# Kernel tuning notes

Measured on AMD Instinct MI355X. Metric: run time of the kernel, lower is better.

## Reference

```python
import jax, jax.numpy as jnp
import numpy as np

S = 8192        # seq_length
H2 = 1024       # 2 * lstm_hidden_size
A = 2048        # attention_hidden_size
E = 768         # embedding_dim == pos_embedding_dim


def _bahdanau_weights(sentence, length, ctx, W_s, b_s, W_c, b_c, v, b_v):
    # sentence: [1, S, H2], ctx: [1, E_ctx]
    u = jnp.einsum('bsh,ha->bsa', sentence, W_s) + b_s \
        + (ctx @ W_c + b_c)[:, None, :]                    # [1, S, A]
    e = jnp.einsum('bsa,a->bs', jnp.tanh(u), v) + b_v       # [1, S]
    mask = jnp.arange(S)[None, :] >= length[:, None]        # [1, S] key mask
    e = jnp.where(mask, -jnp.inf, e)
    all_inf = jnp.all(mask, axis=1)                         # [1]
    # guard fully-masked rows so softmax stays finite, then zero them (matches torch)
    e_safe = jnp.where(all_inf[:, None], jnp.zeros_like(e), e)
    w = jax.nn.softmax(e_safe, axis=1)
    return jnp.where(all_inf[:, None], 0.0, w)              # [1, S]


def setup_inputs() -> dict:
    key = jax.random.key(0)
    ks = jax.random.split(key, 24)
    f = jax.random.normal
    sc_s = 1.0 / np.sqrt(H2)
    sc_c = 1.0 / np.sqrt(E)
    sc_v = 1.0 / np.sqrt(A)
    inp = {
        'sentence': f(ks[0], (1, S, H2), jnp.float32),
        'length': jax.random.randint(ks[1], (1,), 0, S),
        'pos_embedding': f(ks[2], (1, E), jnp.float32),
        'cardinal_phrase_embedding': f(ks[3], (1, E), jnp.float32),
        'headline_embedding': f(ks[4], (1, E), jnp.float32),
    }
    i = 5
    for tag in ('p', 'c', 'h'):
        inp[f'W_sent_{tag}'] = f(ks[i], (H2, A), jnp.float32) * sc_s; i += 1
        inp[f'b_sent_{tag}'] = f(ks[i], (A,), jnp.float32) * sc_s; i += 1
        inp[f'W_ctx_{tag}'] = f(ks[i], (E, A), jnp.float32) * sc_c; i += 1
        inp[f'b_ctx_{tag}'] = f(ks[i], (A,), jnp.float32) * sc_c; i += 1
        inp[f'v_{tag}'] = f(ks[i], (A,), jnp.float32) * sc_v; i += 1
        inp[f'bv_{tag}'] = f(ks[i], (), jnp.float32) * sc_v; i += 1
    return inp


def reference(sentence, length, pos_embedding, cardinal_phrase_embedding,
              headline_embedding,
              W_sent_p, b_sent_p, W_ctx_p, b_ctx_p, v_p, bv_p,
              W_sent_c, b_sent_c, W_ctx_c, b_ctx_c, v_c, bv_c,
              W_sent_h, b_sent_h, W_ctx_h, b_ctx_h, v_h, bv_h):
    w_pos = _bahdanau_weights(sentence, length, pos_embedding,
                              W_sent_p, b_sent_p, W_ctx_p, b_ctx_p, v_p, bv_p)
    w_card = _bahdanau_weights(sentence, length, cardinal_phrase_embedding,
                               W_sent_c, b_sent_c, W_ctx_c, b_ctx_c, v_c, bv_c)
    w_head = _bahdanau_weights(sentence, length, headline_embedding,
                               W_sent_h, b_sent_h, W_ctx_h, b_ctx_h, v_h, bv_h)
    fused = (w_pos + w_card + w_head) / 3.0                 # [1, S]
    return jnp.einsum('bs,bsh->bh', fused, sentence)        # [1, H2]
```

## Files before the change

### kernel.cpp

```cpp
#include <hip/hip_runtime.h>
#include <hip/hip_bf16.h>
#include <stdint.h>


namespace {

constexpr int S = 8192;
constexpr int H = 1024;
constexpr int A = 2048;
constexpr int E = 768;

typedef __bf16 bf16x8 __attribute__((ext_vector_type(8)));
typedef float f32x4 __attribute__((ext_vector_type(4)));

__device__ __forceinline__ void gl_lds16(const void* g, void* l) {
  __builtin_amdgcn_global_load_lds(
      (const __attribute__((address_space(1))) void*)g,
      (__attribute__((address_space(3))) void*)l, 16, 0, 0);
}

__global__ __launch_bounds__(256)
void k_prep(const float* __restrict__ sentence, __bf16* __restrict__ sentB,
            const float* __restrict__ Wp, const float* __restrict__ Wc_s,
            const float* __restrict__ Wh, __bf16* __restrict__ WtB,
            const float* __restrict__ ctx_p, const float* __restrict__ ctx_c,
            const float* __restrict__ ctx_h,
            const float* __restrict__ Wcx_p, const float* __restrict__ Wcx_c,
            const float* __restrict__ Wcx_h,
            const float* __restrict__ bs_p, const float* __restrict__ bs_c,
            const float* __restrict__ bs_h,
            const float* __restrict__ bc_p, const float* __restrict__ bc_c,
            const float* __restrict__ bc_h,
            float* __restrict__ ctxb_q, float* __restrict__ e_arr,
            const int* __restrict__ length, float* __restrict__ out, int n_out) {
  __shared__ float tile[64][65];
  int b = blockIdx.x;
  int t = threadIdx.x;

  if (b < 4096) {
    int len = min(max(length[0], 0), S);
    int lenp = (len + 63) & ~63;
    if (b * 2 >= lenp) return;
    int g = b * 256 + t;
    const float4* s4 = (const float4*)sentence + (size_t)g * 2;
    float4 a = s4[0], c = s4[1];
    bf16x8 o;
    o[0] = (__bf16)a.x; o[1] = (__bf16)a.y; o[2] = (__bf16)a.z; o[3] = (__bf16)a.w;
    o[4] = (__bf16)c.x; o[5] = (__bf16)c.y; o[6] = (__bf16)c.z; o[7] = (__bf16)c.w;
    *((bf16x8*)sentB + g) = o;
  } else if (b < 5632) {
    int r = b - 4096;
    int head = r >> 9; r &= 511;
    const float* W = head == 0 ? Wp : (head == 1 ? Wc_s : Wh);
    __bf16* dst = WtB + (size_t)head * A * H;
    int a0 = (r & 31) * 64;
    int k0 = (r >> 5) * 64;
#pragma unroll
    for (int i = 0; i < 8; ++i) {
      int idx = t + i * 256;
      int rr = idx >> 5;
      int cc = (idx & 31) * 2;
      float2 w2 = *(const float2*)&W[(size_t)(k0 + rr) * A + a0 + cc];
      tile[cc][rr] = w2.x;
      tile[cc + 1][rr] = w2.y;
    }
    __syncthreads();
#pragma unroll
    for (int i = 0; i < 8; ++i) {
      int idx = t + i * 256;
      int al = idx >> 5;
      int kl = (idx & 31) * 2;
      union { ushort2 u; __bf16 h[2]; } o;
      o.h[0] = (__bf16)tile[al][kl];
      o.h[1] = (__bf16)tile[al][kl + 1];
      *(ushort2*)&dst[(size_t)(a0 + al) * H + k0 + kl] = o.u;
    }
  } else if (b < 5728) {
    int r = b - 5632;
    int head = r >> 5;
    int sub = r & 31;
    int ablk = sub & 7;
    int eq = sub >> 3;
    const float* ctx = head == 0 ? ctx_p : (head == 1 ? ctx_c : ctx_h);
    const float* Wc  = head == 0 ? Wcx_p : (head == 1 ? Wcx_c : Wcx_h);
    int a = ablk * 256 + t;
    float s = 0.f;
    if (eq == 0) {
      const float* bs = head == 0 ? bs_p : (head == 1 ? bs_c : bs_h);
      const float* bc = head == 0 ? bc_p : (head == 1 ? bc_c : bc_h);
      s = bs[a] + bc[a];
    }
    int e0 = eq * 192;
#pragma unroll 8
    for (int e = e0; e < e0 + 192; ++e) s = fmaf(ctx[e], Wc[(size_t)e * A + a], s);
    ctxb_q[eq * 3 * A + head * A + a] = s;
  } else {
    int idx = (b - 5728) * 256 + t;
    float4 z = {0.f, 0.f, 0.f, 0.f};
    int total = 6144 + (n_out >> 2);
    for (int i = idx; i < total; i += 2048) {
      if (i < 6144) ((float4*)e_arr)[i] = z;
      else ((float4*)out)[i - 6144] = z;
    }
  }
}

__global__ __launch_bounds__(256)
void k_gemm_e(const __bf16* __restrict__ sentB, const __bf16* __restrict__ WtB,
              const float* __restrict__ ctxb_q,
              const float* __restrict__ v_p, const float* __restrict__ v_c,
              const float* __restrict__ v_h,
              const int* __restrict__ length, float* __restrict__ e_out) {
  int bid = blockIdx.x;
  int xcd = bid & 7;
  int j = bid >> 3;
  int mt = j / 6;
  int pl = j - mt * 6;
  int panel = xcd * 6 + pl;
  int n0 = (panel & 15) * 128;
  int head = panel >> 4;

  int m0 = mt * 64;
  int len = min(max(length[0], 0), S);
  if (m0 >= len) return;
  const float* v  = head == 0 ? v_p : (head == 1 ? v_c : v_h);
  const __bf16* Wt = WtB + (size_t)head * A * H;
  float* e_h = e_out + head * S;

  __shared__ __align__(16) __bf16 lsA[3 * 2048];
  __shared__ __align__(16) __bf16 lsB[3 * 4096];
  __shared__ float e_part[64];

  int tid = threadIdx.x;
  if (tid < 64) e_part[tid] = 0.f;

  int lane = tid & 63;
  int wave = tid >> 6;
  int wm = wave >> 1, wn = wave & 1;
  int quad = lane >> 4, l16 = lane & 15;

  f32x4 acc[2][4];
#pragma unroll
  for (int i = 0; i < 2; ++i)
#pragma unroll
    for (int j2 = 0; j2 < 4; ++j2) acc[i][j2] = (f32x4){0.f, 0.f, 0.f, 0.f};

  const __bf16* gA0 = sentB + (size_t)(m0 + (tid >> 2)) * H + ((tid & 3) * 8);
  const __bf16* gB0 = Wt + (size_t)(n0 + (tid >> 2)) * H + ((tid & 3) * 8);
  const __bf16* gB1 = gB0 + (size_t)64 * H;

#define STAGE(bufi, kk)                                           \
  do {                                                            \
    gl_lds16(gA0 + (kk), lsA + (bufi) * 2048 + tid * 8);          \
    gl_lds16(gB0 + (kk), lsB + (bufi) * 4096 + tid * 8);          \
    gl_lds16(gB1 + (kk), lsB + (bufi) * 4096 + 2048 + tid * 8);   \
  } while (0)

#define COMPUTE(bufi)                                                                          \
  do {                                                                                         \
    bf16x8 af[2], bfv[4];                                                                      \
    _Pragma("unroll")                                                                          \
    for (int i = 0; i < 2; ++i)                                                                \
      af[i] = *(const bf16x8*)&lsA[(bufi) * 2048 + (wm * 32 + i * 16 + l16) * 32 + quad * 8];  \
    _Pragma("unroll")                                                                          \
    for (int jj = 0; jj < 4; ++jj)                                                             \
      bfv[jj] = *(const bf16x8*)&lsB[(bufi) * 4096 + (wn * 64 + jj * 16 + l16) * 32 + quad * 8]; \
    _Pragma("unroll")                                                                          \
    for (int i = 0; i < 2; ++i)                                                                \
      _Pragma("unroll")                                                                        \
      for (int jj = 0; jj < 4; ++jj)                                                           \
        acc[i][jj] = __builtin_amdgcn_mfma_f32_16x16x32_bf16(af[i], bfv[jj], acc[i][jj], 0, 0, 0);\
  } while (0)

  STAGE(0, 0);
  STAGE(1, 32);
  int cur = 0, pf = 2;
#pragma unroll 1
  for (int t = 0; t < 31; ++t) {
    asm volatile("s_waitcnt vmcnt(3)");
    __builtin_amdgcn_s_barrier();
    __builtin_amdgcn_sched_barrier(0);
    if (t < 30) STAGE(pf, (t + 2) * 32);
    COMPUTE(cur);
    cur = cur == 2 ? 0 : cur + 1;
    pf = pf == 2 ? 0 : pf + 1;
  }
  asm volatile("s_waitcnt vmcnt(0)");
  __builtin_amdgcn_s_barrier();
  __builtin_amdgcn_sched_barrier(0);
  COMPUTE(cur);

#undef STAGE
#undef COMPUTE

  float vj[4], cbj[4];
#pragma unroll
  for (int j2 = 0; j2 < 4; ++j2) {
    int col = n0 + wn * 64 + j2 * 16 + l16;
    vj[j2] = v[col];
    cbj[j2] = ctxb_q[head * A + col] + ctxb_q[3 * A + head * A + col] +
              ctxb_q[6 * A + head * A + col] + ctxb_q[9 * A + head * A + col];
  }
#pragma unroll
  for (int i = 0; i < 2; ++i) {
#pragma unroll
    for (int r = 0; r < 4; ++r) {
      float p = 0.f;
#pragma unroll
      for (int j2 = 0; j2 < 4; ++j2) {
        float u = acc[i][j2][r] + cbj[j2];
        float ex = __expf(2.f * u);
        float th = 1.f - 2.f / (ex + 1.f);
        p = fmaf(th, vj[j2], p);
      }
      p += __shfl_xor(p, 1);
      p += __shfl_xor(p, 2);
      p += __shfl_xor(p, 4);
      p += __shfl_xor(p, 8);
      if (l16 == 0) atomicAdd(&e_part[wm * 32 + i * 16 + quad * 4 + r], p);
    }
  }
  __syncthreads();
  if (tid < 64) atomicAdd(&e_h[m0 + tid], e_part[tid]);
}

__global__ void k_stats(const float* __restrict__ e_arr, const int* __restrict__ length,
                        float* __restrict__ stats) {
  int head = blockIdx.x;
  const float* e_h = e_arr + head * S;
  int len = min(max(length[0], 0), S);
  int tid = threadIdx.x;
  __shared__ float red[4];
  __shared__ float bmax;

  float m = -3.4e38f;
  for (int s = tid; s < len; s += 256) m = fmaxf(m, e_h[s]);
#pragma unroll
  for (int o = 32; o >= 1; o >>= 1) m = fmaxf(m, __shfl_xor(m, o));
  if ((tid & 63) == 0) red[tid >> 6] = m;
  __syncthreads();
  if (tid == 0) bmax = fmaxf(fmaxf(red[0], red[1]), fmaxf(red[2], red[3]));
  __syncthreads();
  float mm = bmax;

  float ss = 0.f;
  for (int s = tid; s < len; s += 256) ss += __expf(e_h[s] - mm);
#pragma unroll
  for (int o = 32; o >= 1; o >>= 1) ss += __shfl_xor(ss, o);
  __syncthreads();
  if ((tid & 63) == 0) red[tid >> 6] = ss;
  __syncthreads();
  if (tid == 0) {
    stats[head * 2 + 0] = mm;
    stats[head * 2 + 1] = red[0] + red[1] + red[2] + red[3];
  }
}

__global__ void k_out(const float* __restrict__ sent, const float* __restrict__ e_arr,
                      const float* __restrict__ stats, const int* __restrict__ length,
                      float* __restrict__ out) {
  int len = min(max(length[0], 0), S);
  int r0 = blockIdx.x * 16;
  if (r0 >= len) return;
  int tid = threadIdx.x;

  __shared__ float wrow[16];
  if (tid < 16 && r0 + tid < len) {
    int r = r0 + tid;
    wrow[tid] = (__expf(e_arr[r] - stats[0]) / stats[1] +
                 __expf(e_arr[S + r] - stats[2]) / stats[3] +
                 __expf(e_arr[2 * S + r] - stats[4]) / stats[5]) * (1.f / 3.f);
  }
  __syncthreads();

  int col = tid * 4;
  int rend = min(r0 + 16, len);
  float4 acc = {0.f, 0.f, 0.f, 0.f};
  for (int r = r0; r < rend; ++r) {
    float w = wrow[r - r0];
    float4 x = *(const float4*)(sent + (size_t)r * H + col);
    acc.x = fmaf(w, x.x, acc.x);
    acc.y = fmaf(w, x.y, acc.y);
    acc.z = fmaf(w, x.z, acc.z);
    acc.w = fmaf(w, x.w, acc.w);
  }
  atomicAdd(&out[col + 0], acc.x);
  atomicAdd(&out[col + 1], acc.y);
  atomicAdd(&out[col + 2], acc.z);
  atomicAdd(&out[col + 3], acc.w);
}

}

extern "C" void kernel_launch(void* const* d_in, const int* in_sizes, int n_in,
                              void* d_out, int out_size, void* d_ws, size_t ws_size,
                              hipStream_t stream) {
  const float* sentence = (const float*)d_in[0];
  const int* length     = (const int*)d_in[1];
  const float* ctx_p = (const float*)d_in[2];
  const float* ctx_c = (const float*)d_in[3];
  const float* ctx_h = (const float*)d_in[4];
  const float* W_s[3] = {(const float*)d_in[5],  (const float*)d_in[11], (const float*)d_in[17]};
  const float* b_s[3] = {(const float*)d_in[6],  (const float*)d_in[12], (const float*)d_in[18]};
  const float* W_c[3] = {(const float*)d_in[7],  (const float*)d_in[13], (const float*)d_in[19]};
  const float* b_c[3] = {(const float*)d_in[8],  (const float*)d_in[14], (const float*)d_in[20]};
  const float* v_[3]  = {(const float*)d_in[9],  (const float*)d_in[15], (const float*)d_in[21]};
  float* out = (float*)d_out;

  char* ws = (char*)d_ws;
  __bf16* sentB  = (__bf16*)(ws);
  __bf16* WtB    = (__bf16*)(ws + 16777216);
  float* ctxb_q  = (float*)(ws + 29360128);
  float* e_arr   = (float*)(ws + 29458432);
  float* stats   = (float*)(ws + 29556736);

  k_prep<<<5736, 256, 0, stream>>>(sentence, sentB,
                                   W_s[0], W_s[1], W_s[2], WtB,
                                   ctx_p, ctx_c, ctx_h,
                                   W_c[0], W_c[1], W_c[2],
                                   b_s[0], b_s[1], b_s[2],
                                   b_c[0], b_c[1], b_c[2], ctxb_q, e_arr,
                                   length, out, out_size);
  k_gemm_e<<<6144, 256, 0, stream>>>(sentB, WtB, ctxb_q,
                                     v_[0], v_[1], v_[2], length, e_arr);
  k_stats<<<3, 256, 0, stream>>>(e_arr, length, stats);
  k_out<<<S / 16, 256, 0, stream>>>(sentence, e_arr, stats, length, out);
}
```

Before: 213.5 us.

## Stage GEMM tiles through registers into padded LDS rows

Replaces the direct global-to-LDS async loads with ordinary global loads into registers, followed by explicit LDS stores. The LDS row stride goes from 32 to 40 bf16 elements, a padding meant to cut bank conflicts on the MFMA fragment reads. The K loop is unrolled by three with three register slots to keep global loads in flight one stage ahead. In exchange it uses more VGPRs and LDS and adds extra LDS write instructions, which may reduce occupancy or overlap.

Result: no change. 210.5 us (-1.4%).

```diff
diff --git a/kernel.cpp b/kernel.cpp
--- a/kernel.cpp
+++ b/kernel.cpp
@@ -12,12 +12,6 @@
 
 typedef __bf16 bf16x8 __attribute__((ext_vector_type(8)));
 typedef float f32x4 __attribute__((ext_vector_type(4)));
-
-__device__ __forceinline__ void gl_lds16(const void* g, void* l) {
-  __builtin_amdgcn_global_load_lds(
-      (const __attribute__((address_space(1))) void*)g,
-      (__attribute__((address_space(3))) void*)l, 16, 0, 0);
-}
 
 __global__ __launch_bounds__(256)
 void k_prep(const float* __restrict__ sentence, __bf16* __restrict__ sentB,
@@ -127,8 +121,8 @@
   const __bf16* Wt = WtB + (size_t)head * A * H;
   float* e_h = e_out + head * S;
 
-  __shared__ __align__(16) __bf16 lsA[3 * 2048];
-  __shared__ __align__(16) __bf16 lsB[3 * 4096];
+  __shared__ __align__(16) __bf16 lsA[3 * 2560];
+  __shared__ __align__(16) __bf16 lsB[3 * 5120];
   __shared__ float e_part[64];
 
   int tid = threadIdx.x;
@@ -149,49 +143,76 @@
   const __bf16* gB0 = Wt + (size_t)(n0 + (tid >> 2)) * H + ((tid & 3) * 8);
   const __bf16* gB1 = gB0 + (size_t)64 * H;
 
-#define STAGE(bufi, kk)                                           \
-  do {                                                            \
-    gl_lds16(gA0 + (kk), lsA + (bufi) * 2048 + tid * 8);          \
-    gl_lds16(gB0 + (kk), lsB + (bufi) * 4096 + tid * 8);          \
-    gl_lds16(gB1 + (kk), lsB + (bufi) * 4096 + 2048 + tid * 8);   \
+  int wA  = (tid >> 2) * 40 + (tid & 3) * 8;
+  int wB0 = wA;
+  int wB1 = wA + 64 * 40;
+
+  uint4 s0A, s0B0, s0B1, s1A, s1B0, s1B1, s2A, s2B0, s2B1;
+
+#define LOADB(sl, kk)                             \
+  do {                                            \
+    sl##A  = *(const uint4*)(gA0 + (kk));         \
+    sl##B0 = *(const uint4*)(gB0 + (kk));         \
+    sl##B1 = *(const uint4*)(gB1 + (kk));         \
   } while (0)
 
-#define COMPUTE(bufi)                                                                          \
-  do {                                                                                         \
-    bf16x8 af[2], bfv[4];                                                                      \
-    _Pragma("unroll")                                                                          \
-    for (int i = 0; i < 2; ++i)                                                                \
-      af[i] = *(const bf16x8*)&lsA[(bufi) * 2048 + (wm * 32 + i * 16 + l16) * 32 + quad * 8];  \
-    _Pragma("unroll")                                                                          \
-    for (int jj = 0; jj < 4; ++jj)                                                             \
-      bfv[jj] = *(const bf16x8*)&lsB[(bufi) * 4096 + (wn * 64 + jj * 16 + l16) * 32 + quad * 8]; \
-    _Pragma("unroll")                                                                          \
-    for (int i = 0; i < 2; ++i)                                                                \
-      _Pragma("unroll")                                                                        \
-      for (int jj = 0; jj < 4; ++jj)                                                           \
+#define WRITEB(sl, bufi)                          \
+  do {                                            \
+    *(uint4*)&lsA[(bufi) * 2560 + wA]  = sl##A;   \
+    *(uint4*)&lsB[(bufi) * 5120 + wB0] = sl##B0;  \
+    *(uint4*)&lsB[(bufi) * 5120 + wB1] = sl##B1;  \
+  } while (0)
+
+#define COMPUTE(bufi)                                                                           \
+  do {                                                                                          \
+    bf16x8 af[2], bfv[4];                                                                       \
+    _Pragma("unroll")                                                                           \
+    for (int i = 0; i < 2; ++i)                                                                 \
+      af[i] = *(const bf16x8*)&lsA[(bufi) * 2560 + (wm * 32 + i * 16 + l16) * 40 + quad * 8];   \
+    _Pragma("unroll")                                                                           \
+    for (int jj = 0; jj < 4; ++jj)                                                              \
+      bfv[jj] = *(const bf16x8*)&lsB[(bufi) * 5120 + (wn * 64 + jj * 16 + l16) * 40 + quad * 8];\
+    _Pragma("unroll")                                                                           \
+    for (int i = 0; i < 2; ++i)                                                                 \
+      _Pragma("unroll")                                                                         \
+      for (int jj = 0; jj < 4; ++jj)                                                            \
         acc[i][jj] = __builtin_amdgcn_mfma_f32_16x16x32_bf16(af[i], bfv[jj], acc[i][jj], 0, 0, 0);\
   } while (0)
 
-  STAGE(0, 0);
-  STAGE(1, 32);
-  int cur = 0, pf = 2;
-#pragma unroll 1
-  for (int t = 0; t < 31; ++t) {
-    asm volatile("s_waitcnt vmcnt(3)");
-    __builtin_amdgcn_s_barrier();
-    __builtin_amdgcn_sched_barrier(0);
-    if (t < 30) STAGE(pf, (t + 2) * 32);
-    COMPUTE(cur);
-    cur = cur == 2 ? 0 : cur + 1;
-    pf = pf == 2 ? 0 : pf + 1;
-  }
-  asm volatile("s_waitcnt vmcnt(0)");
+#define ITER(t, sc, bc, sw, bw)                                 \
+  do {                                                          \
+    COMPUTE(bc);                                                \
+    if ((t) <= 28) LOADB(sc, ((t) + 3) * 32);                   \
+    WRITEB(sw, bw);                                             \
+    asm volatile("s_waitcnt lgkmcnt(0)");                       \
+    __builtin_amdgcn_sched_barrier(0);                          \
+    __builtin_amdgcn_s_barrier();                               \
+    __builtin_amdgcn_sched_barrier(0);                          \
+  } while (0)
+
+  LOADB(s0, 0);
+  LOADB(s1, 32);
+  LOADB(s2, 64);
+  WRITEB(s0, 0);
+  WRITEB(s1, 1);
+  asm volatile("s_waitcnt lgkmcnt(0)");
+  __builtin_amdgcn_sched_barrier(0);
   __builtin_amdgcn_s_barrier();
   __builtin_amdgcn_sched_barrier(0);
-  COMPUTE(cur);
-
-#undef STAGE
+
+#pragma unroll 1
+  for (int t = 0; t < 30; t += 3) {
+    ITER(t + 0, s0, 0, s2, 2);
+    ITER(t + 1, s1, 1, s0, 0);
+    ITER(t + 2, s2, 2, s1, 1);
+  }
+  COMPUTE(0);
+  COMPUTE(1);
+
+#undef LOADB
+#undef WRITEB
 #undef COMPUTE
+#undef ITER
 
   float vj[4], cbj[4];
 #pragma unroll
```

## Fuse sentence fp32-to-bf16 conversion into GEMM A-operand loads

Applied to the files above, without the earlier changes.

Removes the separate sentence-to-bf16 conversion pass from the prep kernel and its workspace buffer. The GEMM now loads fp32 sentence rows straight into registers, converts them to bf16 fragments in-loop, and feeds the MFMAs directly, while B still streams through LDS with a 3-buffer pipeline unrolled by 6. This drops a full write and re-read of a 16MB bf16 copy. In exchange each of the 6144 GEMM blocks reads fp32 A (twice the bytes) redundantly across the 48 N-panels, and register pressure rises.

Measured after the change: 270.6 us. 26.7% more time.

```diff
diff --git a/kernel.cpp b/kernel.cpp
--- a/kernel.cpp
+++ b/kernel.cpp
@@ -19,9 +19,15 @@
       (__attribute__((address_space(3))) void*)l, 16, 0, 0);
 }
 
+__device__ __forceinline__ bf16x8 cvt8(float4 lo, float4 hi) {
+  bf16x8 r;
+  r[0] = (__bf16)lo.x; r[1] = (__bf16)lo.y; r[2] = (__bf16)lo.z; r[3] = (__bf16)lo.w;
+  r[4] = (__bf16)hi.x; r[5] = (__bf16)hi.y; r[6] = (__bf16)hi.z; r[7] = (__bf16)hi.w;
+  return r;
+}
+
 __global__ __launch_bounds__(256)
-void k_prep(const float* __restrict__ sentence, __bf16* __restrict__ sentB,
-            const float* __restrict__ Wp, const float* __restrict__ Wc_s,
+void k_prep(const float* __restrict__ Wp, const float* __restrict__ Wc_s,
             const float* __restrict__ Wh, __bf16* __restrict__ WtB,
             const float* __restrict__ ctx_p, const float* __restrict__ ctx_c,
             const float* __restrict__ ctx_h,
@@ -32,24 +38,13 @@
             const float* __restrict__ bc_p, const float* __restrict__ bc_c,
             const float* __restrict__ bc_h,
             float* __restrict__ ctxb_q, float* __restrict__ e_arr,
-            const int* __restrict__ length, float* __restrict__ out, int n_out) {
+            float* __restrict__ out, int n_out) {
   __shared__ float tile[64][65];
   int b = blockIdx.x;
   int t = threadIdx.x;
 
-  if (b < 4096) {
-    int len = min(max(length[0], 0), S);
-    int lenp = (len + 63) & ~63;
-    if (b * 2 >= lenp) return;
-    int g = b * 256 + t;
-    const float4* s4 = (const float4*)sentence + (size_t)g * 2;
-    float4 a = s4[0], c = s4[1];
-    bf16x8 o;
-    o[0] = (__bf16)a.x; o[1] = (__bf16)a.y; o[2] = (__bf16)a.z; o[3] = (__bf16)a.w;
-    o[4] = (__bf16)c.x; o[5] = (__bf16)c.y; o[6] = (__bf16)c.z; o[7] = (__bf16)c.w;
-    *((bf16x8*)sentB + g) = o;
-  } else if (b < 5632) {
-    int r = b - 4096;
+  if (b < 1536) {
+    int r = b;
     int head = r >> 9; r &= 511;
     const float* W = head == 0 ? Wp : (head == 1 ? Wc_s : Wh);
     __bf16* dst = WtB + (size_t)head * A * H;
@@ -75,8 +70,8 @@
       o.h[1] = (__bf16)tile[al][kl + 1];
       *(ushort2*)&dst[(size_t)(a0 + al) * H + k0 + kl] = o.u;
     }
-  } else if (b < 5728) {
-    int r = b - 5632;
+  } else if (b < 1632) {
+    int r = b - 1536;
     int head = r >> 5;
     int sub = r & 31;
     int ablk = sub & 7;
@@ -95,7 +90,7 @@
     for (int e = e0; e < e0 + 192; ++e) s = fmaf(ctx[e], Wc[(size_t)e * A + a], s);
     ctxb_q[eq * 3 * A + head * A + a] = s;
   } else {
-    int idx = (b - 5728) * 256 + t;
+    int idx = (b - 1632) * 256 + t;
     float4 z = {0.f, 0.f, 0.f, 0.f};
     int total = 6144 + (n_out >> 2);
     for (int i = idx; i < total; i += 2048) {
@@ -106,7 +101,7 @@
 }
 
 __global__ __launch_bounds__(256)
-void k_gemm_e(const __bf16* __restrict__ sentB, const __bf16* __restrict__ WtB,
+void k_gemm_e(const float* __restrict__ sent, const __bf16* __restrict__ WtB,
               const float* __restrict__ ctxb_q,
               const float* __restrict__ v_p, const float* __restrict__ v_c,
               const float* __restrict__ v_h,
@@ -127,7 +122,6 @@
   const __bf16* Wt = WtB + (size_t)head * A * H;
   float* e_h = e_out + head * S;
 
-  __shared__ __align__(16) __bf16 lsA[3 * 2048];
   __shared__ __align__(16) __bf16 lsB[3 * 4096];
   __shared__ float e_part[64];
 
@@ -145,53 +139,92 @@
 #pragma unroll
     for (int j2 = 0; j2 < 4; ++j2) acc[i][j2] = (f32x4){0.f, 0.f, 0.f, 0.f};
 
-  const __bf16* gA0 = sentB + (size_t)(m0 + (tid >> 2)) * H + ((tid & 3) * 8);
   const __bf16* gB0 = Wt + (size_t)(n0 + (tid >> 2)) * H + ((tid & 3) * 8);
   const __bf16* gB1 = gB0 + (size_t)64 * H;
-
-#define STAGE(bufi, kk)                                           \
+  const float* gA0 = sent + (size_t)(m0 + wm * 32 + l16) * H + quad * 8;
+  const float* gA1 = gA0 + (size_t)16 * H;
+
+  float4 s0[4], s1[4];
+  bf16x8 ab0, ab1;
+
+#define AISSUE(sl, kk)                              \
+  do {                                              \
+    sl[0] = *(const float4*)(gA0 + (kk));           \
+    sl[1] = *(const float4*)(gA0 + (kk) + 4);       \
+    sl[2] = *(const float4*)(gA1 + (kk));           \
+    sl[3] = *(const float4*)(gA1 + (kk) + 4);       \
+  } while (0)
+
+#define BISSUE(bufi, kk)                                          \
   do {                                                            \
-    gl_lds16(gA0 + (kk), lsA + (bufi) * 2048 + tid * 8);          \
     gl_lds16(gB0 + (kk), lsB + (bufi) * 4096 + tid * 8);          \
     gl_lds16(gB1 + (kk), lsB + (bufi) * 4096 + 2048 + tid * 8);   \
   } while (0)
 
-#define COMPUTE(bufi)                                                                          \
-  do {                                                                                         \
-    bf16x8 af[2], bfv[4];                                                                      \
-    _Pragma("unroll")                                                                          \
-    for (int i = 0; i < 2; ++i)                                                                \
-      af[i] = *(const bf16x8*)&lsA[(bufi) * 2048 + (wm * 32 + i * 16 + l16) * 32 + quad * 8];  \
-    _Pragma("unroll")                                                                          \
-    for (int jj = 0; jj < 4; ++jj)                                                             \
-      bfv[jj] = *(const bf16x8*)&lsB[(bufi) * 4096 + (wn * 64 + jj * 16 + l16) * 32 + quad * 8]; \
-    _Pragma("unroll")                                                                          \
-    for (int i = 0; i < 2; ++i)                                                                \
-      _Pragma("unroll")                                                                        \
-      for (int jj = 0; jj < 4; ++jj)                                                           \
-        acc[i][jj] = __builtin_amdgcn_mfma_f32_16x16x32_bf16(af[i], bfv[jj], acc[i][jj], 0, 0, 0);\
-  } while (0)
-
-  STAGE(0, 0);
-  STAGE(1, 32);
-  int cur = 0, pf = 2;
-#pragma unroll 1
-  for (int t = 0; t < 31; ++t) {
-    asm volatile("s_waitcnt vmcnt(3)");
-    __builtin_amdgcn_s_barrier();
-    __builtin_amdgcn_sched_barrier(0);
-    if (t < 30) STAGE(pf, (t + 2) * 32);
-    COMPUTE(cur);
-    cur = cur == 2 ? 0 : cur + 1;
-    pf = pf == 2 ? 0 : pf + 1;
-  }
-  asm volatile("s_waitcnt vmcnt(0)");
+#define ACVT(sl)                                    \
+  do {                                              \
+    ab0 = cvt8(sl[0], sl[1]);                       \
+    ab1 = cvt8(sl[2], sl[3]);                       \
+  } while (0)
+
+#define COMPUTE(bufi)                                                                           \
+  do {                                                                                          \
+    bf16x8 bfv[4];                                                                              \
+    _Pragma("unroll")                                                                           \
+    for (int jj = 0; jj < 4; ++jj)                                                              \
+      bfv[jj] = *(const bf16x8*)&lsB[(bufi) * 4096 + (wn * 64 + jj * 16 + l16) * 32 + quad * 8];\
+    _Pragma("unroll")                                                                           \
+    for (int jj = 0; jj < 4; ++jj) {                                                            \
+      acc[0][jj] = __builtin_amdgcn_mfma_f32_16x16x32_bf16(ab0, bfv[jj], acc[0][jj], 0, 0, 0);  \
+      acc[1][jj] = __builtin_amdgcn_mfma_f32_16x16x32_bf16(ab1, bfv[jj], acc[1][jj], 0, 0, 0);  \
+    }                                                                                           \
+  } while (0)
+
+#define ITER(t, sIss, sCvt, bufC, bufN)             \
+  do {                                              \
+    AISSUE(sIss, ((t) + 2) * 32);                   \
+    BISSUE(bufN, ((t) + 2) * 32);                   \
+    COMPUTE(bufC);                                  \
+    asm volatile("s_waitcnt vmcnt(6)");             \
+    ACVT(sCvt);                                     \
+    __builtin_amdgcn_sched_barrier(0);              \
+    __builtin_amdgcn_s_barrier();                   \
+    __builtin_amdgcn_sched_barrier(0);              \
+  } while (0)
+
+  AISSUE(s0, 0);
+  BISSUE(0, 0);
+  AISSUE(s1, 32);
+  BISSUE(1, 32);
+  asm volatile("s_waitcnt vmcnt(6)");
+  ACVT(s0);
+  __builtin_amdgcn_sched_barrier(0);
   __builtin_amdgcn_s_barrier();
   __builtin_amdgcn_sched_barrier(0);
-  COMPUTE(cur);
-
-#undef STAGE
+
+#pragma unroll 1
+  for (int r = 0; r < 5; ++r) {
+    int tb = r * 6;
+    ITER(tb + 0, s0, s1, 0, 2);
+    ITER(tb + 1, s1, s0, 1, 0);
+    ITER(tb + 2, s0, s1, 2, 1);
+    ITER(tb + 3, s1, s0, 0, 2);
+    ITER(tb + 4, s0, s1, 1, 0);
+    ITER(tb + 5, s1, s0, 2, 1);
+  }
+  COMPUTE(0);
+  asm volatile("s_waitcnt vmcnt(0)");
+  ACVT(s1);
+  __builtin_amdgcn_sched_barrier(0);
+  __builtin_amdgcn_s_barrier();
+  __builtin_amdgcn_sched_barrier(0);
+  COMPUTE(1);
+
+#undef AISSUE
+#undef BISSUE
+#undef ACVT
 #undef COMPUTE
+#undef ITER
 
   float vj[4], cbj[4];
 #pragma unroll
@@ -308,20 +341,18 @@
   float* out = (float*)d_out;
 
   char* ws = (char*)d_ws;
-  __bf16* sentB  = (__bf16*)(ws);
-  __bf16* WtB    = (__bf16*)(ws + 16777216);
-  float* ctxb_q  = (float*)(ws + 29360128);
-  float* e_arr   = (float*)(ws + 29458432);
-  float* stats   = (float*)(ws + 29556736);
-
-  k_prep<<<5736, 256, 0, stream>>>(sentence, sentB,
-                                   W_s[0], W_s[1], W_s[2], WtB,
+  __bf16* WtB    = (__bf16*)(ws);
+  float* ctxb_q  = (float*)(ws + 12582912);
+  float* e_arr   = (float*)(ws + 12681216);
+  float* stats   = (float*)(ws + 12779520);
+
+  k_prep<<<1640, 256, 0, stream>>>(W_s[0], W_s[1], W_s[2], WtB,
                                    ctx_p, ctx_c, ctx_h,
                                    W_c[0], W_c[1], W_c[2],
                                    b_s[0], b_s[1], b_s[2],
                                    b_c[0], b_c[1], b_c[2], ctxb_q, e_arr,
-                                   length, out, out_size);
-  k_gemm_e<<<6144, 256, 0, stream>>>(sentB, WtB, ctxb_q,
+                                   out, out_size);
+  k_gemm_e<<<6144, 256, 0, stream>>>(sentence, WtB, ctxb_q,
                                      v_[0], v_[1], v_[2], length, e_arr);
   k_stats<<<3, 256, 0, stream>>>(e_arr, length, stats);
   k_out<<<S / 16, 256, 0, stream>>>(sentence, e_arr, stats, length, out);
```

## Pre-pack sentence into MFMA fragment layout and load A operand directly to registers

Applied to the files above, without the earlier changes.

The prep kernel now writes the bf16 sentence in a layout that matches the MFMA A-fragments for each 32-row group and k-tile. The GEMM kernel drops the A tile from shared memory and loads A fragments straight from global memory into registers, using a three-slot register rotation. The main loop is unrolled by three with explicit waitcnt and barrier placement. This removes LDS traffic and LDS reads for A, and shrinks shared memory, at the cost of more VGPRs and uncoalesced-looking but contiguous per-wave global loads. The pipelining behaviour depends on the vmcnt accounting being correct for the mix of register loads and LDS-direct loads.

After: 213.5 us. No clear change (+0.0%).

```diff
diff --git a/kernel.cpp b/kernel.cpp
--- a/kernel.cpp
+++ b/kernel.cpp
@@ -20,7 +20,7 @@
 }
 
 __global__ __launch_bounds__(256)
-void k_prep(const float* __restrict__ sentence, __bf16* __restrict__ sentB,
+void k_prep(const float* __restrict__ sentence, __bf16* __restrict__ packA,
             const float* __restrict__ Wp, const float* __restrict__ Wc_s,
             const float* __restrict__ Wh, __bf16* __restrict__ WtB,
             const float* __restrict__ ctx_p, const float* __restrict__ ctx_c,
@@ -40,14 +40,18 @@
   if (b < 4096) {
     int len = min(max(length[0], 0), S);
     int lenp = (len + 63) & ~63;
-    if (b * 2 >= lenp) return;
-    int g = b * 256 + t;
-    const float4* s4 = (const float4*)sentence + (size_t)g * 2;
-    float4 a = s4[0], c = s4[1];
+    int row = b * 2 + (t >> 7);
+    if (row >= lenp) return;
+    int chunk = t & 127;
+    const float4* s4 = (const float4*)(sentence + (size_t)row * H + chunk * 8);
+    float4 lo = s4[0], hi = s4[1];
     bf16x8 o;
-    o[0] = (__bf16)a.x; o[1] = (__bf16)a.y; o[2] = (__bf16)a.z; o[3] = (__bf16)a.w;
-    o[4] = (__bf16)c.x; o[5] = (__bf16)c.y; o[6] = (__bf16)c.z; o[7] = (__bf16)c.w;
-    *((bf16x8*)sentB + g) = o;
+    o[0] = (__bf16)lo.x; o[1] = (__bf16)lo.y; o[2] = (__bf16)lo.z; o[3] = (__bf16)lo.w;
+    o[4] = (__bf16)hi.x; o[5] = (__bf16)hi.y; o[6] = (__bf16)hi.z; o[7] = (__bf16)hi.w;
+    int g = row >> 5, f = (row >> 4) & 1, l16 = row & 15;
+    int kt = chunk >> 2, quad = chunk & 3;
+    size_t dst = ((size_t)((g * 32 + kt) * 2 + f)) * 512 + (quad * 16 + l16) * 8;
+    *(bf16x8*)(packA + dst) = o;
   } else if (b < 5632) {
     int r = b - 4096;
     int head = r >> 9; r &= 511;
@@ -106,7 +110,7 @@
 }
 
 __global__ __launch_bounds__(256)
-void k_gemm_e(const __bf16* __restrict__ sentB, const __bf16* __restrict__ WtB,
+void k_gemm_e(const __bf16* __restrict__ packA, const __bf16* __restrict__ WtB,
               const float* __restrict__ ctxb_q,
               const float* __restrict__ v_p, const float* __restrict__ v_c,
               const float* __restrict__ v_h,
@@ -127,7 +131,6 @@
   const __bf16* Wt = WtB + (size_t)head * A * H;
   float* e_h = e_out + head * S;
 
-  __shared__ __align__(16) __bf16 lsA[3 * 2048];
   __shared__ __align__(16) __bf16 lsB[3 * 4096];
   __shared__ float e_part[64];
 
@@ -145,53 +148,78 @@
 #pragma unroll
     for (int j2 = 0; j2 < 4; ++j2) acc[i][j2] = (f32x4){0.f, 0.f, 0.f, 0.f};
 
-  const __bf16* gA0 = sentB + (size_t)(m0 + (tid >> 2)) * H + ((tid & 3) * 8);
   const __bf16* gB0 = Wt + (size_t)(n0 + (tid >> 2)) * H + ((tid & 3) * 8);
   const __bf16* gB1 = gB0 + (size_t)64 * H;
-
-#define STAGE(bufi, kk)                                           \
+  const __bf16* gA = packA + ((size_t)(m0 >> 5) + wm) * 32 * 1024 + (size_t)lane * 8;
+
+  bf16x8 a0f0, a0f1, a1f0, a1f1, a2f0, a2f1;
+
+#define AISSUE(sl, kt)                              \
+  do {                                              \
+    sl##f0 = *(const bf16x8*)(gA + (size_t)(kt) * 1024);        \
+    sl##f1 = *(const bf16x8*)(gA + (size_t)(kt) * 1024 + 512);  \
+  } while (0)
+
+#define BISSUE(bufi, kk)                                          \
   do {                                                            \
-    gl_lds16(gA0 + (kk), lsA + (bufi) * 2048 + tid * 8);          \
     gl_lds16(gB0 + (kk), lsB + (bufi) * 4096 + tid * 8);          \
     gl_lds16(gB1 + (kk), lsB + (bufi) * 4096 + 2048 + tid * 8);   \
   } while (0)
 
-#define COMPUTE(bufi)                                                                          \
-  do {                                                                                         \
-    bf16x8 af[2], bfv[4];                                                                      \
-    _Pragma("unroll")                                                                          \
-    for (int i = 0; i < 2; ++i)                                                                \
-      af[i] = *(const bf16x8*)&lsA[(bufi) * 2048 + (wm * 32 + i * 16 + l16) * 32 + quad * 8];  \
-    _Pragma("unroll")                                                                          \
-    for (int jj = 0; jj < 4; ++jj)                                                             \
-      bfv[jj] = *(const bf16x8*)&lsB[(bufi) * 4096 + (wn * 64 + jj * 16 + l16) * 32 + quad * 8]; \
-    _Pragma("unroll")                                                                          \
-    for (int i = 0; i < 2; ++i)                                                                \
-      _Pragma("unroll")                                                                        \
-      for (int jj = 0; jj < 4; ++jj)                                                           \
-        acc[i][jj] = __builtin_amdgcn_mfma_f32_16x16x32_bf16(af[i], bfv[jj], acc[i][jj], 0, 0, 0);\
+#define COMPUTE(sl, bufi)                                                                       \
+  do {                                                                                          \
+    bf16x8 bfv[4];                                                                              \
+    _Pragma("unroll")                                                                           \
+    for (int jj = 0; jj < 4; ++jj)                                                              \
+      bfv[jj] = *(const bf16x8*)&lsB[(bufi) * 4096 + (wn * 64 + jj * 16 + l16) * 32 + quad * 8];\
+    _Pragma("unroll")                                                                           \
+    for (int jj = 0; jj < 4; ++jj) {                                                            \
+      acc[0][jj] = __builtin_amdgcn_mfma_f32_16x16x32_bf16(sl##f0, bfv[jj], acc[0][jj], 0, 0, 0);\
+      acc[1][jj] = __builtin_amdgcn_mfma_f32_16x16x32_bf16(sl##f1, bfv[jj], acc[1][jj], 0, 0, 0);\
+    }                                                                                           \
   } while (0)
 
-  STAGE(0, 0);
-  STAGE(1, 32);
-  int cur = 0, pf = 2;
+#define ITER(t, slI, bufI, slC, bufC)               \
+  do {                                              \
+    AISSUE(slI, (t) + 2);                           \
+    BISSUE(bufI, ((t) + 2) * 32);                   \
+    COMPUTE(slC, bufC);                             \
+    __builtin_amdgcn_sched_barrier(0);              \
+    asm volatile("s_waitcnt vmcnt(4)");             \
+    __builtin_amdgcn_sched_barrier(0);              \
+    __builtin_amdgcn_s_barrier();                   \
+    __builtin_amdgcn_sched_barrier(0);              \
+  } while (0)
+
+  AISSUE(a0, 0);
+  BISSUE(0, 0);
+  AISSUE(a1, 1);
+  BISSUE(1, 32);
+  __builtin_amdgcn_sched_barrier(0);
+  asm volatile("s_waitcnt vmcnt(4)");
+  __builtin_amdgcn_sched_barrier(0);
+  __builtin_amdgcn_s_barrier();
+  __builtin_amdgcn_sched_barrier(0);
+
 #pragma unroll 1
-  for (int t = 0; t < 31; ++t) {
-    asm volatile("s_waitcnt vmcnt(3)");
-    __builtin_amdgcn_s_barrier();
-    __builtin_amdgcn_sched_barrier(0);
-    if (t < 30) STAGE(pf, (t + 2) * 32);
-    COMPUTE(cur);
-    cur = cur == 2 ? 0 : cur + 1;
-    pf = pf == 2 ? 0 : pf + 1;
-  }
+  for (int r = 0; r < 10; ++r) {
+    int tb = r * 3;
+    ITER(tb + 0, a2, 2, a0, 0);
+    ITER(tb + 1, a0, 0, a1, 1);
+    ITER(tb + 2, a1, 1, a2, 2);
+  }
+  COMPUTE(a0, 0);
+  __builtin_amdgcn_sched_barrier(0);
   asm volatile("s_waitcnt vmcnt(0)");
+  __builtin_amdgcn_sched_barrier(0);
   __builtin_amdgcn_s_barrier();
   __builtin_amdgcn_sched_barrier(0);
-  COMPUTE(cur);
-
-#undef STAGE
+  COMPUTE(a1, 1);
+
+#undef AISSUE
+#undef BISSUE
 #undef COMPUTE
+#undef ITER
 
   float vj[4], cbj[4];
 #pragma unroll
@@ -308,20 +336,20 @@
   float* out = (float*)d_out;
 
   char* ws = (char*)d_ws;
-  __bf16* sentB  = (__bf16*)(ws);
+  __bf16* packA  = (__bf16*)(ws);
   __bf16* WtB    = (__bf16*)(ws + 16777216);
   float* ctxb_q  = (float*)(ws + 29360128);
   float* e_arr   = (float*)(ws + 29458432);
   float* stats   = (float*)(ws + 29556736);
 
-  k_prep<<<5736, 256, 0, stream>>>(sentence, sentB,
+  k_prep<<<5736, 256, 0, stream>>>(sentence, packA,
                                    W_s[0], W_s[1], W_s[2], WtB,
                                    ctx_p, ctx_c, ctx_h,
                                    W_c[0], W_c[1], W_c[2],
                                    b_s[0], b_s[1], b_s[2],
                                    b_c[0], b_c[1], b_c[2], ctxb_q, e_arr,
                                    length, out, out_size);
-  k_gemm_e<<<6144, 256, 0, stream>>>(sentB, WtB, ctxb_q,
+  k_gemm_e<<<6144, 256, 0, stream>>>(packA, WtB, ctxb_q,
                                      v_[0], v_[1], v_[2], length, e_arr);
   k_stats<<<3, 256, 0, stream>>>(e_arr, length, stats);
   k_out<<<S / 16, 256, 0, stream>>>(sentence, e_arr, stats, length, out);
```
